# Optimization experiments

Measured on AMD Instinct MI355X. Metric: run time of the kernel, lower is better.

The kernel has to match this reference:

```python
import jax, jax.numpy as jnp
import numpy as np

N_LOC, CONTENT, ADDR, HID, IN, OUT = 32768, 512, 64, 1024, 256, 10
OVERALL = CONTENT + ADDR   # 576
GRU_IN = IN + OVERALL      # 832
EPS = 1e-7


def setup_inputs() -> dict:
    key = jax.random.key(0)
    ks = jax.random.split(key, 16)
    def w(i, shape, scale=0.02):
        return jax.random.normal(ks[i], shape, jnp.float32) * scale
    return {
        "x": jax.random.normal(ks[0], (IN, 1), jnp.float32),
        "h0": jnp.zeros((HID, 1), jnp.float32),
        "memory_contents": w(1, (N_LOC, CONTENT)),
        "memory_addresses": w(2, (N_LOC, ADDR)),
        "W_query": w(3, (OVERALL, HID)),
        "b_query": jnp.zeros((OVERALL, 1), jnp.float32),
        "u_sharpen": w(4, (1, HID)),
        "b_sharpen": jnp.zeros((1, 1), jnp.float32),
        "u_lru": w(5, (1, HID)),
        "b_lru": jnp.zeros((1, 1), jnp.float32),
        "W_erase": w(6, (CONTENT, HID)),
        "b_erase": jnp.zeros((CONTENT, 1), jnp.float32),
        "W_content_hidden": w(7, (CONTENT, HID)),
        "W_content_input": w(8, (CONTENT, IN)),
        "b_content": jnp.zeros((CONTENT, 1), jnp.float32),
        "W_ih": w(9, (3 * HID, GRU_IN)),
        "W_hh": w(10, (3 * HID, HID)),
        "b_ih": jnp.zeros((3 * HID,), jnp.float32),
        "b_hh": jnp.zeros((3 * HID,), jnp.float32),
        "W_output": w(11, (OUT, HID)),
        "b_output": jnp.zeros((OUT, 1), jnp.float32),
        "num_addressing_steps": 8,
    }


def _dntm_forward(x, h0, memory_contents, memory_addresses, W_query, b_query,
                  u_sharpen, b_sharpen, u_lru, b_lru, W_erase, b_erase,
                  W_content_hidden, W_content_input, b_content,
                  W_ih, W_hh, b_ih, b_hh, W_output, b_output, num_steps):
    addr_norm_sq = jnp.sum(memory_addresses * memory_addresses, axis=1)  # (N,) constant across steps
    xcol = x[:, 0]

    def step(carry, _):
        h, mem, ema = carry  # h: (HID,1), mem: (N,CONTENT), ema: (N,)
        # --- address memory (content-based, sharpened, LRU-gated) ---
        query = (W_query @ h + b_query)[:, 0]                        # (OVERALL,)
        beta = jax.nn.softplus(u_sharpen @ h + b_sharpen)[0, 0] + 1.0
        full = jnp.concatenate([mem, memory_addresses], axis=1)      # (N, OVERALL) full memory view
        dots = full @ query                                          # (N,)
        row_norm = jnp.sqrt(jnp.sum(mem * mem, axis=1) + addr_norm_sq)
        sim = beta * dots / (row_norm * jnp.linalg.norm(query) + EPS)  # sharpened cosine sim (N,)
        gamma = jax.nn.sigmoid(u_lru @ h + b_lru)[0, 0]
        w_addr = jax.nn.softmax(sim - gamma * ema)                   # (N,)
        ema_new = 0.1 * ema + 0.9 * sim
        # --- read ---
        reading = full.T @ w_addr                                    # (OVERALL,)
        # --- GRU controller step (torch GRUCell math) ---
        gi = W_ih @ jnp.concatenate([xcol, reading]) + b_ih          # (3*HID,)
        gh = W_hh @ h[:, 0] + b_hh
        r = jax.nn.sigmoid(gi[:HID] + gh[:HID])
        z = jax.nn.sigmoid(gi[HID:2 * HID] + gh[HID:2 * HID])
        n = jnp.tanh(gi[2 * HID:] + r * gh[2 * HID:])
        h_new = ((1.0 - z) * n + z * h[:, 0])[:, None]               # (HID,1)
        # --- write/update memory: rank-1 erase + rank-1 add ---
        erase = jax.nn.sigmoid(W_erase @ h_new + b_erase)[:, 0]      # (CONTENT,)
        cand = jax.nn.relu(W_content_hidden @ h_new + W_content_input @ x + b_content)[:, 0]
        mem_new = mem * (1.0 - w_addr[:, None] * erase[None, :]) + w_addr[:, None] * cand[None, :]
        return (h_new, mem_new, ema_new), None

    ema0 = jnp.zeros((N_LOC,), memory_contents.dtype)
    (h, _, _), _ = jax.lax.scan(step, (h0, memory_contents, ema0), None, length=num_steps)
    output = jax.nn.log_softmax(W_output @ h + b_output, axis=0)     # (OUT,1)
    return h, output


def reference(x, h0, memory_contents, memory_addresses, W_query, b_query,
              u_sharpen, b_sharpen, u_lru, b_lru, W_erase, b_erase,
              W_content_hidden, W_content_input, b_content,
              W_ih, W_hh, b_ih, b_hh, W_output, b_output, num_addressing_steps):
    return _dntm_forward(x, h0, memory_contents, memory_addresses, W_query, b_query,
                         u_sharpen, b_sharpen, u_lru, b_lru, W_erase, b_erase,
                         W_content_hidden, W_content_input, b_content,
                         W_ih, W_hh, b_ih, b_hh, W_output, b_output, num_addressing_steps)
```

## Files before the change

### kernel.cpp

```cpp
#include <hip/hip_runtime.h>
#include <math.h>

#define N_LOC 32768
#define CONTENT 512
#define ADDR_D 64
#define HID 1024
#define IN_D 256
#define OUT_D 10
#define OVERALL 576
#define GRU_IN 832
#define EPS_C 1e-7f
#define NSTEPS 8

#define NBLK_P 2048
#define NWAVE_P (NBLK_P * 4)
#define RCOLS (OVERALL + 1)
#define RP 580
#define RSP 580

__device__ __forceinline__ float wred(float v) {
    #pragma unroll
    for (int m = 32; m; m >>= 1) v += __shfl_xor(v, m, 64);
    return v;
}
__device__ __forceinline__ float sigm(float x) { return 1.0f / (1.0f + expf(-x)); }
__device__ __forceinline__ float dot4(float4 a, float4 b) {
    return a.x * b.x + a.y * b.y + a.z * b.z + a.w * b.w;
}

__global__ __launch_bounds__(256) void k_init(const float* __restrict__ addrRows,
                                              float* __restrict__ addrsq,
                                              float* __restrict__ ema) {
    int tid = threadIdx.x, wid = tid >> 6, lane = tid & 63;
    int gid = blockIdx.x * 256 + tid;
    if (gid < N_LOC) ema[gid] = 0.0f;
    for (int i = blockIdx.x * 4 + wid; i < N_LOC; i += gridDim.x * 4) {
        float a = addrRows[(size_t)i * ADDR_D + lane];
        float sq = wred(a * a);
        if (lane == 0) addrsq[i] = sq;
    }
}

__global__ __launch_bounds__(256) void k_small(
    const float* __restrict__ W_e, const float* __restrict__ b_e,
    const float* __restrict__ W_ch, const float* __restrict__ W_ci, const float* __restrict__ b_c,
    const float* __restrict__ W_q, const float* __restrict__ b_q,
    const float* __restrict__ u_s, const float* __restrict__ u_l,
    const float* __restrict__ x, const float* __restrict__ h,
    float* __restrict__ erase, float* __restrict__ cand, float* __restrict__ query,
    float* __restrict__ slots_t, int doEC) {
    int tid = threadIdx.x, wid = tid >> 6, lane = tid & 63;
    int r = blockIdx.x;
    __shared__ float red[4];

    int role, rr;
    if (doEC) {
        if (r < CONTENT)                { role = 0; rr = r; }
        else if (r < 2 * CONTENT)       { role = 1; rr = r - CONTENT; }
        else if (r < 2 * CONTENT + OVERALL) { role = 2; rr = r - 2 * CONTENT; }
        else                            { role = 3 + (r - (2 * CONTENT + OVERALL)); rr = 0; }
    } else {
        if (r < OVERALL)                { role = 2; rr = r; }
        else                            { role = 3 + (r - OVERALL); rr = 0; }
    }

    const float4* h4 = (const float4*)h;
    const float4* row4;
    if (role == 0)      row4 = (const float4*)(W_e  + (size_t)rr * HID);
    else if (role == 1) row4 = (const float4*)(W_ch + (size_t)rr * HID);
    else if (role == 2) row4 = (const float4*)(W_q  + (size_t)rr * HID);
    else if (role == 3) row4 = (const float4*)u_s;
    else                row4 = (const float4*)u_l;

    float d = dot4(row4[tid], h4[tid]);
    if (role == 1 && tid < 64) {
        const float4* ci4 = (const float4*)(W_ci + (size_t)rr * IN_D);
        d += dot4(ci4[tid], ((const float4*)x)[tid]);
    }
    d = wred(d);
    if (lane == 0) red[wid] = d;
    __syncthreads();
    if (tid == 0) {
        float s = red[0] + red[1] + red[2] + red[3];
        if (role == 0)      erase[rr] = sigm(s + b_e[rr]);
        else if (role == 1) cand[rr]  = fmaxf(s + b_c[rr], 0.0f);
        else if (role == 2) query[rr] = s + b_q[rr];
        else if (role == 3) slots_t[1] = s;
        else                slots_t[2] = s;
    }
}

__global__ __launch_bounds__(256) void k_passAB(
    const float* __restrict__ memC,
    const float* __restrict__ addrRows, const float* __restrict__ query,
    const float* __restrict__ eraseAll, const float* __restrict__ candAll,
    const float* __restrict__ addrsq, float* __restrict__ ema,
    const float* __restrict__ expAll, float* __restrict__ exp_t,
    float* __restrict__ part, const float* __restrict__ rsAll,
    const float* __restrict__ slots_t,
    const float* __restrict__ b_sh, const float* __restrict__ b_lr,
    int tstep) {
    int tid = threadIdx.x, wid = tid >> 6, lane = tid & 63;
    int gw = blockIdx.x * 4 + wid;
    const int i0 = gw;
    const int i1 = gw + NWAVE_P;
    const int i2 = gw + 2 * NWAVE_P;
    const int i3 = gw + 3 * NWAVE_P;

    __shared__ __align__(16) float lredw[4][RP];

    const float4* r0p = (const float4*)(memC + (size_t)i0 * CONTENT);
    const float4* r1p = (const float4*)(memC + (size_t)i1 * CONTENT);
    const float4* r2p = (const float4*)(memC + (size_t)i2 * CONTENT);
    const float4* r3p = (const float4*)(memC + (size_t)i3 * CONTENT);
    float4 m00 = r0p[lane], m01 = r0p[64 + lane];
    float4 m10 = r1p[lane], m11 = r1p[64 + lane];
    float4 m20 = r2p[lane], m21 = r2p[64 + lane];
    float4 m30 = r3p[lane], m31 = r3p[64 + lane];
    float av0 = addrRows[(size_t)i0 * ADDR_D + lane];
    float av1 = addrRows[(size_t)i1 * ADDR_D + lane];
    float av2 = addrRows[(size_t)i2 * ADDR_D + lane];
    float av3 = addrRows[(size_t)i3 * ADDR_D + lane];
    float eo0 = ema[i0], eo1 = ema[i1], eo2 = ema[i2], eo3 = ema[i3];
    float asq0 = addrsq[i0], asq1 = addrsq[i1], asq2 = addrsq[i2], asq3 = addrsq[i3];

    const float4 q0 = *(const float4*)(query + 4 * lane);
    const float4 q1 = *(const float4*)(query + 256 + 4 * lane);
    const float qa = query[512 + lane];
    const float qq = wred(dot4(q0, q0) + dot4(q1, q1) + qa * qa);
    const float qnorm = sqrtf(qq);
    const float bs = slots_t[1] + b_sh[0];
    const float beta = (bs > 20.0f ? bs : log1pf(expf(bs))) + 1.0f;
    const float gamma = sigm(slots_t[2] + b_lr[0]);

    #define UPD(m, e, c, wv) \
        m.x = m.x * (1.0f - wv * e.x) + wv * c.x; \
        m.y = m.y * (1.0f - wv * e.y) + wv * c.y; \
        m.z = m.z * (1.0f - wv * e.z) + wv * c.z; \
        m.w = m.w * (1.0f - wv * e.w) + wv * c.w;
    for (int u = 0; u < tstep; u++) {
        const float4 e0 = *(const float4*)(eraseAll + (size_t)u * CONTENT + 4 * lane);
        const float4 e1 = *(const float4*)(eraseAll + (size_t)u * CONTENT + 256 + 4 * lane);
        const float4 c0 = *(const float4*)(candAll + (size_t)u * CONTENT + 4 * lane);
        const float4 c1 = *(const float4*)(candAll + (size_t)u * CONTENT + 256 + 4 * lane);
        const float invp = 1.0f / rsAll[(size_t)u * RSP + OVERALL];
        const float* eb = expAll + (size_t)u * N_LOC;
        const float wv0 = eb[i0] * invp;
        const float wv1 = eb[i1] * invp;
        const float wv2 = eb[i2] * invp;
        const float wv3 = eb[i3] * invp;
        UPD(m00, e0, c0, wv0) UPD(m01, e1, c1, wv0)
        UPD(m10, e0, c0, wv1) UPD(m11, e1, c1, wv1)
        UPD(m20, e0, c0, wv2) UPD(m21, e1, c1, wv2)
        UPD(m30, e0, c0, wv3) UPD(m31, e1, c1, wv3)
    }
    #undef UPD

    float d0 = dot4(m00, q0) + dot4(m01, q1) + av0 * qa;
    float d1 = dot4(m10, q0) + dot4(m11, q1) + av1 * qa;
    float d2 = dot4(m20, q0) + dot4(m21, q1) + av2 * qa;
    float d3 = dot4(m30, q0) + dot4(m31, q1) + av3 * qa;
    float s0 = dot4(m00, m00) + dot4(m01, m01);
    float s1 = dot4(m10, m10) + dot4(m11, m11);
    float s2 = dot4(m20, m20) + dot4(m21, m21);
    float s3 = dot4(m30, m30) + dot4(m31, m31);
    #pragma unroll
    for (int m = 32; m; m >>= 1) {
        d0 += __shfl_xor(d0, m, 64); s0 += __shfl_xor(s0, m, 64);
        d1 += __shfl_xor(d1, m, 64); s1 += __shfl_xor(s1, m, 64);
        d2 += __shfl_xor(d2, m, 64); s2 += __shfl_xor(s2, m, 64);
        d3 += __shfl_xor(d3, m, 64); s3 += __shfl_xor(s3, m, 64);
    }
    float sim0 = beta * d0 / (sqrtf(s0 + asq0) * qnorm + EPS_C);
    float sim1 = beta * d1 / (sqrtf(s1 + asq1) * qnorm + EPS_C);
    float sim2 = beta * d2 / (sqrtf(s2 + asq2) * qnorm + EPS_C);
    float sim3 = beta * d3 / (sqrtf(s3 + asq3) * qnorm + EPS_C);
    float es0 = expf(sim0 - gamma * eo0);
    float es1 = expf(sim1 - gamma * eo1);
    float es2 = expf(sim2 - gamma * eo2);
    float es3 = expf(sim3 - gamma * eo3);
    if (lane == 0) {
        ema[i0] = 0.1f * eo0 + 0.9f * sim0;
        ema[i1] = 0.1f * eo1 + 0.9f * sim1;
        ema[i2] = 0.1f * eo2 + 0.9f * sim2;
        ema[i3] = 0.1f * eo3 + 0.9f * sim3;
        exp_t[i0] = es0; exp_t[i1] = es1; exp_t[i2] = es2; exp_t[i3] = es3;
    }

    float* lw = lredw[wid];
    #pragma unroll
    for (int k = 0; k < 4; k++) {
        float a = (k == 0) ? (es0 * m00.x + es1 * m10.x + es2 * m20.x + es3 * m30.x)
                : (k == 1) ? (es0 * m00.y + es1 * m10.y + es2 * m20.y + es3 * m30.y)
                : (k == 2) ? (es0 * m00.z + es1 * m10.z + es2 * m20.z + es3 * m30.z)
                           : (es0 * m00.w + es1 * m10.w + es2 * m20.w + es3 * m30.w);
        lw[4 * lane + k] = a;
        float b2 = (k == 0) ? (es0 * m01.x + es1 * m11.x + es2 * m21.x + es3 * m31.x)
                 : (k == 1) ? (es0 * m01.y + es1 * m11.y + es2 * m21.y + es3 * m31.y)
                 : (k == 2) ? (es0 * m01.z + es1 * m11.z + es2 * m21.z + es3 * m31.z)
                            : (es0 * m01.w + es1 * m11.w + es2 * m21.w + es3 * m31.w);
        lw[256 + 4 * lane + k] = b2;
    }
    lw[512 + lane] = es0 * av0 + es1 * av1 + es2 * av2 + es3 * av3;
    if (lane == 0) lw[576] = es0 + es1 + es2 + es3;
    __syncthreads();

    float* pb = part + (size_t)blockIdx.x * RP;
    for (int c = tid; c < RCOLS; c += 256)
        pb[c] = lredw[0][c] + lredw[1][c] + lredw[2][c] + lredw[3][c];
}

__global__ __launch_bounds__(256) void k_redf(const float* __restrict__ part,
                                              float* __restrict__ rs) {
    int tid = threadIdx.x;
    int cl = tid & 15;
    int r0 = tid >> 4;
    int c = blockIdx.x * 16 + cl;
    __shared__ float lds[16][17];
    float acc = 0.0f;
    if (c < RCOLS) {
        #pragma unroll 8
        for (int r = r0; r < NBLK_P; r += 16)
            acc += part[(size_t)r * RP + c];
    }
    lds[r0][cl] = acc;
    __syncthreads();
    if (tid < 16) {
        int cc = blockIdx.x * 16 + tid;
        if (cc < RCOLS) {
            float s = 0.0f;
            #pragma unroll
            for (int g = 0; g < 16; g++) s += lds[g][tid];
            rs[cc] = s;
        }
    }
}

__global__ __launch_bounds__(256) void k_gru(
    const float* __restrict__ W_ih, const float* __restrict__ W_hh,
    const float* __restrict__ b_ih, const float* __restrict__ b_hh,
    const float* __restrict__ x, const float* __restrict__ rs,
    const float* __restrict__ hcur, float* __restrict__ hnew) {
    int tid = threadIdx.x, wid = tid >> 6, lane = tid & 63;
    const int k = blockIdx.x;
    __shared__ float red[4][6];

    const float invs = 1.0f / rs[OVERALL];
    const float4* Wi0 = (const float4*)(W_ih + (size_t)k * GRU_IN);
    const float4* Wi1 = (const float4*)(W_ih + (size_t)(k + HID) * GRU_IN);
    const float4* Wi2 = (const float4*)(W_ih + (size_t)(k + 2 * HID) * GRU_IN);
    const float4* Wh0 = (const float4*)(W_hh + (size_t)k * HID);
    const float4* Wh1 = (const float4*)(W_hh + (size_t)(k + HID) * HID);
    const float4* Wh2 = (const float4*)(W_hh + (size_t)(k + 2 * HID) * HID);

    float gi0 = 0, gi1 = 0, gi2 = 0;
    if (tid < GRU_IN / 4) {
        float4 v;
        if (tid < IN_D / 4) v = ((const float4*)x)[tid];
        else {
            v = ((const float4*)rs)[tid - IN_D / 4];
            v.x *= invs; v.y *= invs; v.z *= invs; v.w *= invs;
        }
        gi0 = dot4(Wi0[tid], v); gi1 = dot4(Wi1[tid], v); gi2 = dot4(Wi2[tid], v);
    }
    float4 hv = ((const float4*)hcur)[tid];
    float gh0 = dot4(Wh0[tid], hv);
    float gh1 = dot4(Wh1[tid], hv);
    float gh2 = dot4(Wh2[tid], hv);

    #pragma unroll
    for (int m = 32; m; m >>= 1) {
        gi0 += __shfl_xor(gi0, m, 64); gi1 += __shfl_xor(gi1, m, 64); gi2 += __shfl_xor(gi2, m, 64);
        gh0 += __shfl_xor(gh0, m, 64); gh1 += __shfl_xor(gh1, m, 64); gh2 += __shfl_xor(gh2, m, 64);
    }
    if (lane == 0) {
        red[wid][0] = gi0; red[wid][1] = gi1; red[wid][2] = gi2;
        red[wid][3] = gh0; red[wid][4] = gh1; red[wid][5] = gh2;
    }
    __syncthreads();
    if (tid == 0) {
        float a0 = red[0][0] + red[1][0] + red[2][0] + red[3][0];
        float a1 = red[0][1] + red[1][1] + red[2][1] + red[3][1];
        float a2 = red[0][2] + red[1][2] + red[2][2] + red[3][2];
        float a3 = red[0][3] + red[1][3] + red[2][3] + red[3][3];
        float a4 = red[0][4] + red[1][4] + red[2][4] + red[3][4];
        float a5 = red[0][5] + red[1][5] + red[2][5] + red[3][5];
        float r = sigm(a0 + b_ih[k] + a3 + b_hh[k]);
        float z = sigm(a1 + b_ih[HID + k] + a4 + b_hh[HID + k]);
        float n = tanhf(a2 + b_ih[2 * HID + k] + r * (a5 + b_hh[2 * HID + k]));
        hnew[k] = (1.0f - z) * n + z * hcur[k];
    }
}

__global__ __launch_bounds__(256) void k_out(const float* __restrict__ W_o,
                                             const float* __restrict__ b_o,
                                             const float* __restrict__ h,
                                             float* __restrict__ out) {
    int tid = threadIdx.x, wid = tid >> 6, lane = tid & 63;
    __shared__ float lg[OUT_D];
    for (int j = tid; j < HID; j += 256) out[j] = h[j];
    const float4* h4 = (const float4*)h;
    for (int u = wid; u < OUT_D; u += 4) {
        const float4* row = (const float4*)(W_o + (size_t)u * HID);
        float d = 0.0f;
        #pragma unroll
        for (int i = 0; i < 4; i++) d += dot4(row[lane + 64 * i], h4[lane + 64 * i]);
        d = wred(d);
        if (lane == 0) lg[u] = d + b_o[u];
    }
    __syncthreads();
    if (tid == 0) {
        float m = -1e30f;
        for (int u = 0; u < OUT_D; u++) m = fmaxf(m, lg[u]);
        float se = 0.0f;
        for (int u = 0; u < OUT_D; u++) se += expf(lg[u] - m);
        float lse = m + logf(se);
        for (int u = 0; u < OUT_D; u++) out[HID + u] = lg[u] - lse;
    }
}

extern "C" void kernel_launch(void* const* d_in, const int* in_sizes, int n_in,
                              void* d_out, int out_size, void* d_ws, size_t ws_size,
                              hipStream_t stream) {
    const float* x    = (const float*)d_in[0];
    const float* h0   = (const float*)d_in[1];
    const float* memC = (const float*)d_in[2];
    const float* addrR= (const float*)d_in[3];
    const float* W_q  = (const float*)d_in[4];
    const float* b_q  = (const float*)d_in[5];
    const float* u_s  = (const float*)d_in[6];
    const float* b_s  = (const float*)d_in[7];
    const float* u_l  = (const float*)d_in[8];
    const float* b_l  = (const float*)d_in[9];
    const float* W_e  = (const float*)d_in[10];
    const float* b_e  = (const float*)d_in[11];
    const float* W_ch = (const float*)d_in[12];
    const float* W_ci = (const float*)d_in[13];
    const float* b_c  = (const float*)d_in[14];
    const float* W_ih = (const float*)d_in[15];
    const float* W_hh = (const float*)d_in[16];
    const float* b_ih = (const float*)d_in[17];
    const float* b_hh = (const float*)d_in[18];
    const float* W_o  = (const float*)d_in[19];
    const float* b_o  = (const float*)d_in[20];

    const size_t SM_ADDRSQ = 0;
    const size_t SM_EXPA   = SM_ADDRSQ + N_LOC;
    const size_t SM_EMA    = SM_EXPA + (size_t)NSTEPS * N_LOC;
    const size_t SM_QUERY  = SM_EMA + N_LOC;
    const size_t SM_ER     = SM_QUERY + NSTEPS * OVERALL;
    const size_t SM_CAND   = SM_ER + NSTEPS * CONTENT;
    const size_t SM_H      = SM_CAND + NSTEPS * CONTENT;
    const size_t SM_SLOTS  = SM_H + (NSTEPS + 1) * HID;
    const size_t SM_RS     = SM_SLOTS + NSTEPS * 8;
    const size_t SM_PART   = SM_RS + (size_t)NSTEPS * RSP;

    float* sb = (float*)d_ws;
    float* addrsq  = sb + SM_ADDRSQ;
    float* exp_all = sb + SM_EXPA;
    float* ema     = sb + SM_EMA;
    float* query   = sb + SM_QUERY;
    float* erase   = sb + SM_ER;
    float* cand    = sb + SM_CAND;
    float* H       = sb + SM_H;
    float* slots   = sb + SM_SLOTS;
    float* rsAll   = sb + SM_RS;
    float* part    = sb + SM_PART;

    k_init<<<512, 256, 0, stream>>>(addrR, addrsq, ema);
    k_small<<<OVERALL + 2, 256, 0, stream>>>(
        W_e, b_e, W_ch, W_ci, b_c, W_q, b_q, u_s, u_l, x, h0,
        erase, cand, query, slots, 0);

    const float* hcur = h0;
    for (int t = 0; t < NSTEPS; t++) {
        k_passAB<<<NBLK_P, 256, 0, stream>>>(
            memC, addrR,
            query + t * OVERALL,
            erase, cand,
            addrsq, ema,
            exp_all, exp_all + (size_t)t * N_LOC,
            part, rsAll,
            slots + t * 8, b_s, b_l,
            t);
        float* rs_t = rsAll + (size_t)t * RSP;
        k_redf<<<(RCOLS + 15) / 16, 256, 0, stream>>>(part, rs_t);
        float* hn = H + (t + 1) * HID;
        k_gru<<<HID, 256, 0, stream>>>(W_ih, W_hh, b_ih, b_hh, x,
                                       rs_t, hcur, hn);
        if (t < NSTEPS - 1) {
            k_small<<<2 * CONTENT + OVERALL + 2, 256, 0, stream>>>(
                W_e, b_e, W_ch, W_ci, b_c, W_q, b_q, u_s, u_l, x, hn,
                erase + t * CONTENT, cand + t * CONTENT,
                query + (t + 1) * OVERALL, slots + (t + 1) * 8, 1);
        }
        hcur = hn;
    }
    k_out<<<1, 256, 0, stream>>>(W_o, b_o, hcur, (float*)d_out);
}
```

Baseline: 547.7 us.

## Precompute step-invariant x projections, vectorize LDS stores, reparallelize partial reduction

Adds a one-time kernel that computes W_ih[:, :IN]·x and W_content_input·x once, so the per-step GRU and candidate kernels no longer reread those weight columns. The passAB partial writes to LDS become float4 stores. k_redf now uses one block per column, with 256 threads striding over 2048 partial rows and a wave reduction, replacing 16 columns per block. The per-column reduction reads strided rows, so its coalescing is worse. The precompute adds one extra launch.

```diff
diff --git a/kernel.cpp b/kernel.cpp
--- a/kernel.cpp
+++ b/kernel.cpp
@@ -41,12 +41,31 @@
     }
 }
 
+__global__ __launch_bounds__(64) void k_pre(const float* __restrict__ W_ih,
+                                            const float* __restrict__ W_ci,
+                                            const float* __restrict__ x,
+                                            float* __restrict__ gix,
+                                            float* __restrict__ cix) {
+    int tid = threadIdx.x;
+    int r = blockIdx.x;
+    const float4* x4 = (const float4*)x;
+    const float4* row;
+    if (r < 3 * HID) row = (const float4*)(W_ih + (size_t)r * GRU_IN);
+    else             row = (const float4*)(W_ci + (size_t)(r - 3 * HID) * IN_D);
+    float d = dot4(row[tid], x4[tid]);
+    d = wred(d);
+    if (tid == 0) {
+        if (r < 3 * HID) gix[r] = d;
+        else             cix[r - 3 * HID] = d;
+    }
+}
+
 __global__ __launch_bounds__(256) void k_small(
     const float* __restrict__ W_e, const float* __restrict__ b_e,
-    const float* __restrict__ W_ch, const float* __restrict__ W_ci, const float* __restrict__ b_c,
+    const float* __restrict__ W_ch, const float* __restrict__ cix, const float* __restrict__ b_c,
     const float* __restrict__ W_q, const float* __restrict__ b_q,
     const float* __restrict__ u_s, const float* __restrict__ u_l,
-    const float* __restrict__ x, const float* __restrict__ h,
+    const float* __restrict__ h,
     float* __restrict__ erase, float* __restrict__ cand, float* __restrict__ query,
     float* __restrict__ slots_t, int doEC) {
     int tid = threadIdx.x, wid = tid >> 6, lane = tid & 63;
@@ -73,17 +92,13 @@
     else                row4 = (const float4*)u_l;
 
     float d = dot4(row4[tid], h4[tid]);
-    if (role == 1 && tid < 64) {
-        const float4* ci4 = (const float4*)(W_ci + (size_t)rr * IN_D);
-        d += dot4(ci4[tid], ((const float4*)x)[tid]);
-    }
     d = wred(d);
     if (lane == 0) red[wid] = d;
     __syncthreads();
     if (tid == 0) {
         float s = red[0] + red[1] + red[2] + red[3];
         if (role == 0)      erase[rr] = sigm(s + b_e[rr]);
-        else if (role == 1) cand[rr]  = fmaxf(s + b_c[rr], 0.0f);
+        else if (role == 1) cand[rr]  = fmaxf(s + cix[rr] + b_c[rr], 0.0f);
         else if (role == 2) query[rr] = s + b_q[rr];
         else if (role == 3) slots_t[1] = s;
         else                slots_t[2] = s;
@@ -188,19 +203,18 @@
     }
 
     float* lw = lredw[wid];
-    #pragma unroll
-    for (int k = 0; k < 4; k++) {
-        float a = (k == 0) ? (es0 * m00.x + es1 * m10.x + es2 * m20.x + es3 * m30.x)
-                : (k == 1) ? (es0 * m00.y + es1 * m10.y + es2 * m20.y + es3 * m30.y)
-                : (k == 2) ? (es0 * m00.z + es1 * m10.z + es2 * m20.z + es3 * m30.z)
-                           : (es0 * m00.w + es1 * m10.w + es2 * m20.w + es3 * m30.w);
-        lw[4 * lane + k] = a;
-        float b2 = (k == 0) ? (es0 * m01.x + es1 * m11.x + es2 * m21.x + es3 * m31.x)
-                 : (k == 1) ? (es0 * m01.y + es1 * m11.y + es2 * m21.y + es3 * m31.y)
-                 : (k == 2) ? (es0 * m01.z + es1 * m11.z + es2 * m21.z + es3 * m31.z)
-                            : (es0 * m01.w + es1 * m11.w + es2 * m21.w + es3 * m31.w);
-        lw[256 + 4 * lane + k] = b2;
-    }
+    float4 va = make_float4(
+        es0 * m00.x + es1 * m10.x + es2 * m20.x + es3 * m30.x,
+        es0 * m00.y + es1 * m10.y + es2 * m20.y + es3 * m30.y,
+        es0 * m00.z + es1 * m10.z + es2 * m20.z + es3 * m30.z,
+        es0 * m00.w + es1 * m10.w + es2 * m20.w + es3 * m30.w);
+    *(float4*)(lw + 4 * lane) = va;
+    float4 vb = make_float4(
+        es0 * m01.x + es1 * m11.x + es2 * m21.x + es3 * m31.x,
+        es0 * m01.y + es1 * m11.y + es2 * m21.y + es3 * m31.y,
+        es0 * m01.z + es1 * m11.z + es2 * m21.z + es3 * m31.z,
+        es0 * m01.w + es1 * m11.w + es2 * m21.w + es3 * m31.w);
+    *(float4*)(lw + 256 + 4 * lane) = vb;
     lw[512 + lane] = es0 * av0 + es1 * av1 + es2 * av2 + es3 * av3;
     if (lane == 0) lw[576] = es0 + es1 + es2 + es3;
     __syncthreads();
@@ -212,55 +226,40 @@
 
 __global__ __launch_bounds__(256) void k_redf(const float* __restrict__ part,
                                               float* __restrict__ rs) {
-    int tid = threadIdx.x;
-    int cl = tid & 15;
-    int r0 = tid >> 4;
-    int c = blockIdx.x * 16 + cl;
-    __shared__ float lds[16][17];
+    int tid = threadIdx.x, wid = tid >> 6, lane = tid & 63;
+    int c = blockIdx.x;
+    __shared__ float red[4];
     float acc = 0.0f;
-    if (c < RCOLS) {
-        #pragma unroll 8
-        for (int r = r0; r < NBLK_P; r += 16)
-            acc += part[(size_t)r * RP + c];
-    }
-    lds[r0][cl] = acc;
+    #pragma unroll
+    for (int j = 0; j < NBLK_P / 256; j++)
+        acc += part[(size_t)(tid + 256 * j) * RP + c];
+    acc = wred(acc);
+    if (lane == 0) red[wid] = acc;
     __syncthreads();
-    if (tid < 16) {
-        int cc = blockIdx.x * 16 + tid;
-        if (cc < RCOLS) {
-            float s = 0.0f;
-            #pragma unroll
-            for (int g = 0; g < 16; g++) s += lds[g][tid];
-            rs[cc] = s;
-        }
-    }
+    if (tid == 0) rs[c] = red[0] + red[1] + red[2] + red[3];
 }
 
 __global__ __launch_bounds__(256) void k_gru(
     const float* __restrict__ W_ih, const float* __restrict__ W_hh,
     const float* __restrict__ b_ih, const float* __restrict__ b_hh,
-    const float* __restrict__ x, const float* __restrict__ rs,
+    const float* __restrict__ gix, const float* __restrict__ rs,
     const float* __restrict__ hcur, float* __restrict__ hnew) {
     int tid = threadIdx.x, wid = tid >> 6, lane = tid & 63;
     const int k = blockIdx.x;
     __shared__ float red[4][6];
 
     const float invs = 1.0f / rs[OVERALL];
-    const float4* Wi0 = (const float4*)(W_ih + (size_t)k * GRU_IN);
-    const float4* Wi1 = (const float4*)(W_ih + (size_t)(k + HID) * GRU_IN);
-    const float4* Wi2 = (const float4*)(W_ih + (size_t)(k + 2 * HID) * GRU_IN);
+    const float4* Wi0 = (const float4*)(W_ih + (size_t)k * GRU_IN + IN_D);
+    const float4* Wi1 = (const float4*)(W_ih + (size_t)(k + HID) * GRU_IN + IN_D);
+    const float4* Wi2 = (const float4*)(W_ih + (size_t)(k + 2 * HID) * GRU_IN + IN_D);
     const float4* Wh0 = (const float4*)(W_hh + (size_t)k * HID);
     const float4* Wh1 = (const float4*)(W_hh + (size_t)(k + HID) * HID);
     const float4* Wh2 = (const float4*)(W_hh + (size_t)(k + 2 * HID) * HID);
 
     float gi0 = 0, gi1 = 0, gi2 = 0;
-    if (tid < GRU_IN / 4) {
-        float4 v;
-        if (tid < IN_D / 4) v = ((const float4*)x)[tid];
-        else {
-            v = ((const float4*)rs)[tid - IN_D / 4];
-            v.x *= invs; v.y *= invs; v.z *= invs; v.w *= invs;
-        }
+    if (tid < OVERALL / 4) {
+        float4 v = ((const float4*)rs)[tid];
+        v.x *= invs; v.y *= invs; v.z *= invs; v.w *= invs;
         gi0 = dot4(Wi0[tid], v); gi1 = dot4(Wi1[tid], v); gi2 = dot4(Wi2[tid], v);
     }
     float4 hv = ((const float4*)hcur)[tid];
@@ -279,9 +278,9 @@
     }
     __syncthreads();
     if (tid == 0) {
-        float a0 = red[0][0] + red[1][0] + red[2][0] + red[3][0];
-        float a1 = red[0][1] + red[1][1] + red[2][1] + red[3][1];
-        float a2 = red[0][2] + red[1][2] + red[2][2] + red[3][2];
+        float a0 = red[0][0] + red[1][0] + red[2][0] + red[3][0] + gix[k];
+        float a1 = red[0][1] + red[1][1] + red[2][1] + red[3][1] + gix[HID + k];
+        float a2 = red[0][2] + red[1][2] + red[2][2] + red[3][2] + gix[2 * HID + k];
         float a3 = red[0][3] + red[1][3] + red[2][3] + red[3][3];
         float a4 = red[0][4] + red[1][4] + red[2][4] + red[3][4];
         float a5 = red[0][5] + red[1][5] + red[2][5] + red[3][5];
@@ -353,7 +352,9 @@
     const size_t SM_H      = SM_CAND + NSTEPS * CONTENT;
     const size_t SM_SLOTS  = SM_H + (NSTEPS + 1) * HID;
     const size_t SM_RS     = SM_SLOTS + NSTEPS * 8;
-    const size_t SM_PART   = SM_RS + (size_t)NSTEPS * RSP;
+    const size_t SM_GIX    = SM_RS + (size_t)NSTEPS * RSP;
+    const size_t SM_CIX    = SM_GIX + 3 * HID;
+    const size_t SM_PART   = SM_CIX + CONTENT;
 
     float* sb = (float*)d_ws;
     float* addrsq  = sb + SM_ADDRSQ;
@@ -365,11 +366,14 @@
     float* H       = sb + SM_H;
     float* slots   = sb + SM_SLOTS;
     float* rsAll   = sb + SM_RS;
+    float* gix     = sb + SM_GIX;
+    float* cix     = sb + SM_CIX;
     float* part    = sb + SM_PART;
 
     k_init<<<512, 256, 0, stream>>>(addrR, addrsq, ema);
+    k_pre<<<3 * HID + CONTENT, 64, 0, stream>>>(W_ih, W_ci, x, gix, cix);
     k_small<<<OVERALL + 2, 256, 0, stream>>>(
-        W_e, b_e, W_ch, W_ci, b_c, W_q, b_q, u_s, u_l, x, h0,
+        W_e, b_e, W_ch, cix, b_c, W_q, b_q, u_s, u_l, h0,
         erase, cand, query, slots, 0);
 
     const float* hcur = h0;
@@ -384,13 +388,13 @@
             slots + t * 8, b_s, b_l,
             t);
         float* rs_t = rsAll + (size_t)t * RSP;
-        k_redf<<<(RCOLS + 15) / 16, 256, 0, stream>>>(part, rs_t);
+        k_redf<<<RCOLS, 256, 0, stream>>>(part, rs_t);
         float* hn = H + (t + 1) * HID;
-        k_gru<<<HID, 256, 0, stream>>>(W_ih, W_hh, b_ih, b_hh, x,
+        k_gru<<<HID, 256, 0, stream>>>(W_ih, W_hh, b_ih, b_hh, gix,
                                        rs_t, hcur, hn);
         if (t < NSTEPS - 1) {
             k_small<<<2 * CONTENT + OVERALL + 2, 256, 0, stream>>>(
-                W_e, b_e, W_ch, W_ci, b_c, W_q, b_q, u_s, u_l, x, hn,
+                W_e, b_e, W_ch, cix, b_c, W_q, b_q, u_s, u_l, hn,
                 erase + t * CONTENT, cand + t * CONTENT,
                 query + (t + 1) * OVERALL, slots + (t + 1) * 8, 1);
         }
```

Result: faster. 489.6 us, median of 2 (-10.6%).
